# Kernel tuning notes

Measured on AMD Instinct MI355X. Metric: run time of the kernel, lower is better.

Reference implementation:

```python
import jax, jax.numpy as jnp
import numpy as np

B, N, E = 64, 2048, 32768
F_IN, NHID, RULES = 256, 512, 128
RATIO = 0.5
K1 = int(np.ceil(RATIO * N)); K2 = int(np.ceil(RATIO * K1)); K3 = int(np.ceil(RATIO * K2))


def _gcn(x, src, dst, em, W, b):
    # GCNConv with self-loops and symmetric normalization; em is a float edge-validity mask.
    n = x.shape[0]
    h = x @ W  # [n, out]
    deg = jax.ops.segment_sum(em, dst, num_segments=n) + 1.0  # in-degree + self-loop
    dinv = jax.lax.rsqrt(deg)
    coef = dinv[src] * dinv[dst] * em  # [E]
    agg = jax.ops.segment_sum(h[src] * coef[:, None], dst, num_segments=n)
    return agg + h / deg[:, None] + b  # second term = self-loop with norm 1/deg


def _sag_pool(x, src, dst, em, Wg, bg, k):
    # SAGPooling: GCN scorer, per-graph top-k, scale kept nodes by tanh(score), filter+reindex edges.
    n = x.shape[0]
    score = _gcn(x, src, dst, em, Wg, bg)[:, 0]  # [n]
    vals, perm = jax.lax.top_k(score, k)
    xk = x[perm] * jnp.tanh(vals)[:, None]  # [k, F]
    newidx = jnp.full((n,), -1, dtype=src.dtype).at[perm].set(jnp.arange(k, dtype=src.dtype))
    ns, nd = newidx[src], newidx[dst]
    keep = em * (ns >= 0).astype(em.dtype) * (nd >= 0).astype(em.dtype)
    return xk, jnp.maximum(ns, 0), jnp.maximum(nd, 0), keep


_gcn_b = jax.vmap(_gcn, in_axes=(0, 0, 0, 0, None, None))
_pool_b = jax.vmap(_sag_pool, in_axes=(0, 0, 0, 0, None, None, None))


def setup_inputs() -> dict:
    key = jax.random.key(0)
    ks = jax.random.split(key, 16)
    def w(k, shape, fan_in):
        return jax.random.normal(k, shape, jnp.float32) * (1.0 / np.sqrt(fan_in))
    return {
        "x": jax.random.normal(ks[0], (B, N, F_IN), jnp.float32),
        "src": jax.random.randint(ks[1], (B, E), 0, N, jnp.int32),
        "dst": jax.random.randint(ks[2], (B, E), 0, N, jnp.int32),
        "W1": w(ks[3], (F_IN, NHID), F_IN), "b1": jnp.zeros((NHID,), jnp.float32),
        "Wp1": w(ks[4], (NHID, 1), NHID), "bp1": jnp.zeros((1,), jnp.float32),
        "W2": w(ks[5], (NHID, NHID), NHID), "b2": jnp.zeros((NHID,), jnp.float32),
        "Wp2": w(ks[6], (NHID, 1), NHID), "bp2": jnp.zeros((1,), jnp.float32),
        "W3": w(ks[7], (NHID, NHID), NHID), "b3": jnp.zeros((NHID,), jnp.float32),
        "Wp3": w(ks[8], (NHID, 1), NHID), "bp3": jnp.zeros((1,), jnp.float32),
        "lin1_W": w(ks[9], (2 * NHID, NHID), 2 * NHID), "lin1_b": jnp.zeros((NHID,), jnp.float32),
        "lin2_W": w(ks[10], (NHID, NHID // 2), NHID), "lin2_b": jnp.zeros((NHID // 2,), jnp.float32),
        "pi_W": w(ks[11], (NHID // 2, RULES), NHID // 2), "pi_b": jnp.zeros((RULES,), jnp.float32),
        "v_W": w(ks[12], (NHID // 2, 1), NHID // 2), "v_b": jnp.zeros((1,), jnp.float32),
    }


def reference(x, src, dst, W1, b1, Wp1, bp1, W2, b2, Wp2, bp2, W3, b3, Wp3, bp3,
              lin1_W, lin1_b, lin2_W, lin2_b, pi_W, pi_b, v_W, v_b):
    em = jnp.ones(src.shape, x.dtype)
    h = jax.nn.relu(_gcn_b(x, src, dst, em, W1, b1))
    h, s, d, em = _pool_b(h, src, dst, em, Wp1, bp1, K1)
    x1 = jnp.concatenate([h.max(axis=1), h.mean(axis=1)], axis=1)  # [B, 2*NHID]
    h = jax.nn.relu(_gcn_b(h, s, d, em, W2, b2))
    h, s, d, em = _pool_b(h, s, d, em, Wp2, bp2, K2)
    x2 = jnp.concatenate([h.max(axis=1), h.mean(axis=1)], axis=1)
    h = jax.nn.relu(_gcn_b(h, s, d, em, W3, b3))
    h, s, d, em = _pool_b(h, s, d, em, Wp3, bp3, K3)
    x3 = jnp.concatenate([h.max(axis=1), h.mean(axis=1)], axis=1)
    z = x1 + x2 + x3
    z = jax.nn.relu(z @ lin1_W + lin1_b)
    z = jax.nn.relu(z @ lin2_W + lin2_b)
    pi = jax.nn.log_softmax(z @ pi_W + pi_b, axis=1)
    v = jax.nn.relu(z @ v_W + v_b)
    return pi, v
```

## Files before the change

kernel.cpp:

```cpp
#include <hip/hip_runtime.h>
#include <math.h>
#include <cstdint>

#define B_   64
#define N_   2048
#define E_   32768
#define FIN  256
#define H_   512

typedef __bf16 bf16x8 __attribute__((ext_vector_type(8)));
typedef float  f32x4  __attribute__((ext_vector_type(4)));

__device__ __forceinline__ unsigned short f2bf(float f) {
  unsigned u = __float_as_uint(f);
  u += 0x7FFF + ((u >> 16) & 1);
  return (unsigned short)(u >> 16);
}
__device__ __forceinline__ unsigned pk2(float a, float b) {
  return (unsigned)f2bf(a) | ((unsigned)f2bf(b) << 16);
}
__device__ __forceinline__ float bflo(unsigned u) { return __uint_as_float(u << 16); }
__device__ __forceinline__ float bfhi(unsigned u) { return __uint_as_float(u & 0xFFFF0000u); }

__device__ __forceinline__ void accum8(float* acc, uint4 u, float c) {
  acc[0] += c * bflo(u.x); acc[1] += c * bfhi(u.x);
  acc[2] += c * bflo(u.y); acc[3] += c * bfhi(u.y);
  acc[4] += c * bflo(u.z); acc[5] += c * bfhi(u.z);
  acc[6] += c * bflo(u.w); acc[7] += c * bfhi(u.w);
}

__device__ __forceinline__ void glds16(const void* g, void* l) {
  __builtin_amdgcn_global_load_lds(
      (const __attribute__((address_space(1))) unsigned int*)g,
      (__attribute__((address_space(3))) unsigned int*)l, 16, 0, 0);
}

__global__ void xcvt_k(const float* __restrict__ x, unsigned short* __restrict__ xb) {
  int i = blockIdx.x * 256 + threadIdx.x;
  float4 f = reinterpret_cast<const float4*>(x)[i];
  uint2 o; o.x = pk2(f.x, f.y); o.y = pk2(f.z, f.w);
  reinterpret_cast<uint2*>(xb)[i] = o;
}

__global__ void wcvt_k(const float* __restrict__ W, unsigned short* __restrict__ Wt, int K) {
  int idx = blockIdx.x * 256 + threadIdx.x;
  int k = idx >> 9, n = idx & 511;
  Wt[n * K + k] = f2bf(W[idx]);
}

__global__ __launch_bounds__(256) void gemm_mfma(
    const unsigned short* __restrict__ Xb,
    const int* __restrict__ perm, const float* __restrict__ tanhv,
    const unsigned short* __restrict__ Wt, unsigned short* __restrict__ Y,
    int K, int kl2, int nsl2,
    const float* __restrict__ bias, const float* __restrict__ wp, float* __restrict__ hs) {
  __shared__ uint4 As[512];
  __shared__ uint4 Bs[512];
  const int tid = threadIdx.x;
  const int w = tid >> 6, L = tid & 63;
  const int bid = blockIdx.x;
  const int xcd = bid & 7;
  const int t = bid >> 3;
  const int colb = t & 3;
  const int strip = ((t >> 2) << 3) + xcd;
  const int m0 = strip * 128;
  const int n0 = colb * 128;
  const int e = L & 15, q = L >> 4;

  const int sw3 = (L >> 3) & 7;
  const int cA = (w * 64 + L) ^ sw3;
  const int rloc = cA >> 2;
  const int kcs = (cA & 3) * 8;

  f32x4 acc[4][4];
#pragma unroll
  for (int j = 0; j < 4; j++)
#pragma unroll
    for (int nn = 0; nn < 4; nn++) acc[j][nn] = (f32x4){0.f, 0.f, 0.f, 0.f};

  size_t asrc[2];
#pragma unroll
  for (int i = 0; i < 2; i++) {
    int g = m0 + i * 64 + rloc;
    size_t row;
    if (perm) {
      int b = g >> kl2;
      int node = perm[g];
      row = (size_t)(b << nsl2) + node;
    } else {
      row = (size_t)g;
    }
    asrc[i] = row * (size_t)K + kcs;
  }
  size_t bsrc[2];
#pragma unroll
  for (int i = 0; i < 2; i++) bsrc[i] = (size_t)(n0 + i * 64 + rloc) * K + kcs;

  const int fo = e * 4 + q;
  const int fosw = fo ^ (fo >> 3);

  for (int k0 = 0; k0 < K; k0 += 32) {
    glds16(Xb + asrc[0] + k0, &As[0 * 256 + w * 64]);
    glds16(Xb + asrc[1] + k0, &As[1 * 256 + w * 64]);
    glds16(Wt + bsrc[0] + k0, &Bs[0 * 256 + w * 64]);
    glds16(Wt + bsrc[1] + k0, &Bs[1 * 256 + w * 64]);
    __syncthreads();
    bf16x8 af[4], bfr[4];
#pragma unroll
    for (int j = 0; j < 4; j++) af[j]  = __builtin_bit_cast(bf16x8, As[((w & 1) * 4 + j) * 64 + fosw]);
#pragma unroll
    for (int j = 0; j < 4; j++) bfr[j] = __builtin_bit_cast(bf16x8, Bs[((w >> 1) * 4 + j) * 64 + fosw]);
#pragma unroll
    for (int j = 0; j < 4; j++)
#pragma unroll
      for (int nn = 0; nn < 4; nn++)
        acc[j][nn] = __builtin_amdgcn_mfma_f32_16x16x32_bf16(af[j], bfr[nn], acc[j][nn], 0, 0, 0);
    __syncthreads();
  }
  float bs[4], wsv[4];
#pragma unroll
  for (int nn = 0; nn < 4; nn++) {
    int coly = n0 + ((w >> 1) * 4 + nn) * 16 + e;
    bs[nn]  = bias ? bias[coly] : 0.f;
    wsv[nn] = wp ? wp[coly] : 0.f;
  }
#pragma unroll
  for (int j = 0; j < 4; j++) {
    int mt = (w & 1) * 4 + j;
#pragma unroll
    for (int r = 0; r < 4; r++) {
      int grow = m0 + mt * 16 + q * 4 + r;
      float t2 = tanhv ? tanhv[grow] : 1.0f;
      float p = 0.f;
#pragma unroll
      for (int nn = 0; nn < 4; nn++) {
        int coly = n0 + ((w >> 1) * 4 + nn) * 16 + e;
        float v = acc[j][nn][r] * t2;
        if (bias) v = fmaxf(v + bs[nn], 0.f);
        Y[(size_t)grow * 512 + coly] = f2bf(v);
        p += v * wsv[nn];
      }
      if (wp) {
        p += __shfl_xor(p, 1, 64); p += __shfl_xor(p, 2, 64);
        p += __shfl_xor(p, 4, 64); p += __shfl_xor(p, 8, 64);
        if ((L & 15) == 0) atomicAdd(&hs[grow], p);
      }
    }
  }
}

__global__ void count_k(const int* __restrict__ dst, int* __restrict__ cnt, int nl2) {
  int g = blockIdx.x * 256 + threadIdx.x;
  int d = dst[g];
  if (d < 0) return;
  int b = g >> 15;
  atomicAdd(&cnt[(b << nl2) + d], 1);
}

__global__ __launch_bounds__(256) void scan_k(const int* __restrict__ cnt,
                                              int* __restrict__ rowptr, int* __restrict__ cursor,
                                              float* __restrict__ deg, float* __restrict__ dinv, int n) {
  int b = blockIdx.x, tid = threadIdx.x;
  __shared__ int ls[2048];
  __shared__ int ch[256];
  int per = n >> 8;
  int base = tid * per;
  int s = 0;
  for (int i = 0; i < per; i++) { int v = cnt[b * n + base + i]; ls[base + i] = v; s += v; }
  ch[tid] = s;
  __syncthreads();
  for (int off = 1; off < 256; off <<= 1) {
    int v = (tid >= off) ? ch[tid - off] : 0;
    __syncthreads();
    ch[tid] += v;
    __syncthreads();
  }
  int run = (tid == 0) ? 0 : ch[tid - 1];
  for (int i = 0; i < per; i++) {
    int v = ls[base + i];
    rowptr[b * (n + 1) + base + i] = run;
    cursor[b * n + base + i] = run;
    float d = (float)(v + 1);
    deg[b * n + base + i] = d;
    dinv[b * n + base + i] = 1.0f / sqrtf(d);
    run += v;
  }
  if (tid == 255) rowptr[b * (n + 1) + n] = run;
}

__global__ void fill_k(const int* __restrict__ src, const int* __restrict__ dst,
                       const float* __restrict__ dinv, int* cursor, int* col,
                       float* ce, int nl2) {
  int g = blockIdx.x * 256 + threadIdx.x;
  int d = dst[g];
  if (d < 0) return;
  int b = g >> 15;
  int s = src[g];
  int pos = atomicAdd(&cursor[(b << nl2) + d], 1);
  col[(b << 15) + pos] = s;
  ce[(b << 15) + pos] = dinv[(b << nl2) + s] * dinv[(b << nl2) + d];
}

__global__ __launch_bounds__(256) void aggx_k(
    const unsigned short* __restrict__ X,
    const int* __restrict__ rowptr, const int* __restrict__ col,
    const float* __restrict__ ce, const float* __restrict__ deg,
    unsigned short* __restrict__ Xa) {
  const int w = threadIdx.x >> 6, L = threadIdx.x & 63;
  const int xcd = blockIdx.x & 7;
  const int slot = blockIdx.x >> 3;
  const int gslot = slot >> 9;
  const int v4 = slot & 511;
  const int b = (gslot << 3) + xcd;
  const int v = v4 * 4 + w;
  const int bbase = b << 11;
  const int vg = bbase + v;
  const int rb = b * (N_ + 1) + v;
  const int st = rowptr[rb], en = rowptr[rb + 1];
  const int* cb = col + (b << 15);
  const float* cee = ce + (b << 15);
  const int h = L >> 5, hl = L & 31;
  const unsigned short* Xb_ = X + (size_t)bbase * 256 + hl * 8;
  const int T = en - st + 1;
  const float selfc = 1.0f / deg[vg];
  float acc[8] = {0.f, 0.f, 0.f, 0.f, 0.f, 0.f, 0.f, 0.f};
  for (int t = h; t < T; t += 2) {
    bool isE = (t < T - 1);
    int s = isE ? cb[st + t] : v;
    float c = isE ? cee[st + t] : selfc;
    uint4 u = *(const uint4*)(Xb_ + (size_t)s * 256);
    accum8(acc, u, c);
  }
#pragma unroll
  for (int i = 0; i < 8; i++) acc[i] += __shfl_xor(acc[i], 32, 64);
  if (h == 0) {
    uint4 o;
    o.x = pk2(acc[0], acc[1]); o.y = pk2(acc[2], acc[3]);
    o.z = pk2(acc[4], acc[5]); o.w = pk2(acc[6], acc[7]);
    *(uint4*)(Xa + (size_t)vg * 256 + hl * 8) = o;
  }
}

template <int NL2>
__global__ __launch_bounds__(256) void agg_k(
    const unsigned short* __restrict__ H,
    const int* __restrict__ rowptr, const int* __restrict__ col,
    const float* __restrict__ ce, const float* __restrict__ deg,
    const float* __restrict__ bias, const float* __restrict__ wp,
    unsigned short* __restrict__ C, float* __restrict__ hs) {
  const int n = 1 << NL2;
  const int xcd = blockIdx.x & 7;
  const int slot = blockIdx.x >> 3;
  const int gslot = slot >> (NL2 - 2);
  const int v4 = slot & ((1 << (NL2 - 2)) - 1);
  const int b = (gslot << 3) + xcd;
  const int w = threadIdx.x >> 6, L = threadIdx.x & 63;
  const int v = v4 * 4 + w;
  const int bbase = b << NL2;
  const int vg = bbase + v;
  const int rb = b * (n + 1) + v;
  const int st = rowptr[rb], en = rowptr[rb + 1];
  const int* cb = col + (b << 15);
  const float* cee = ce + (b << 15);
  const unsigned short* Hb_ = H + (size_t)bbase * 512 + (size_t)L * 8;

  float acc[8] = {0.f, 0.f, 0.f, 0.f, 0.f, 0.f, 0.f, 0.f};
  int e2 = st;
  for (; e2 + 4 <= en; e2 += 4) {
    int s0 = cb[e2], s1 = cb[e2 + 1], s2 = cb[e2 + 2], s3 = cb[e2 + 3];
    float c0 = cee[e2], c1 = cee[e2 + 1], c2 = cee[e2 + 2], c3 = cee[e2 + 3];
    uint4 u0 = *(const uint4*)(Hb_ + (size_t)s0 * 512);
    uint4 u1 = *(const uint4*)(Hb_ + (size_t)s1 * 512);
    uint4 u2 = *(const uint4*)(Hb_ + (size_t)s2 * 512);
    uint4 u3 = *(const uint4*)(Hb_ + (size_t)s3 * 512);
    accum8(acc, u0, c0); accum8(acc, u1, c1);
    accum8(acc, u2, c2); accum8(acc, u3, c3);
  }
  for (; e2 < en; e2++) {
    int s = cb[e2];
    uint4 u = *(const uint4*)(Hb_ + (size_t)s * 512);
    accum8(acc, u, cee[e2]);
  }
  {
    float idg = 1.0f / deg[vg];
    uint4 u = *(const uint4*)(Hb_ + (size_t)v * 512);
    accum8(acc, u, idg);
  }
  float4 bLo = *(const float4*)(bias + L * 8);
  float4 bHi = *(const float4*)(bias + L * 8 + 4);
  acc[0] = fmaxf(acc[0] + bLo.x, 0.f); acc[1] = fmaxf(acc[1] + bLo.y, 0.f);
  acc[2] = fmaxf(acc[2] + bLo.z, 0.f); acc[3] = fmaxf(acc[3] + bLo.w, 0.f);
  acc[4] = fmaxf(acc[4] + bHi.x, 0.f); acc[5] = fmaxf(acc[5] + bHi.y, 0.f);
  acc[6] = fmaxf(acc[6] + bHi.z, 0.f); acc[7] = fmaxf(acc[7] + bHi.w, 0.f);
  uint4 o;
  o.x = pk2(acc[0], acc[1]); o.y = pk2(acc[2], acc[3]);
  o.z = pk2(acc[4], acc[5]); o.w = pk2(acc[6], acc[7]);
  *(uint4*)(C + (size_t)vg * 512 + L * 8) = o;
  float4 wLo = *(const float4*)(wp + L * 8);
  float4 wHi = *(const float4*)(wp + L * 8 + 4);
  float p = acc[0] * wLo.x + acc[1] * wLo.y + acc[2] * wLo.z + acc[3] * wLo.w
          + acc[4] * wHi.x + acc[5] * wHi.y + acc[6] * wHi.z + acc[7] * wHi.w;
#pragma unroll
  for (int off = 32; off > 0; off >>= 1) p += __shfl_down(p, off, 64);
  if (L == 0) hs[vg] = p;
}

__global__ void scoreagg_k(const float* __restrict__ hs, const int* __restrict__ rowptr,
                           const int* __restrict__ col, const float* __restrict__ ce,
                           const float* __restrict__ deg, const float* __restrict__ bp,
                           float* __restrict__ score, int nl2) {
  int idx = blockIdx.x * 256 + threadIdx.x;
  int n = 1 << nl2;
  int b = idx >> nl2, v = idx & (n - 1);
  int rb = b * (n + 1) + v;
  int st = rowptr[rb], en = rowptr[rb + 1];
  const int* cb = col + (b << 15);
  const float* cee = ce + (b << 15);
  int bbase = b << nl2;
  float acc = 0.f;
  int e = st;
  for (; e + 4 <= en; e += 4) {
    acc += hs[bbase + cb[e]] * cee[e] + hs[bbase + cb[e + 1]] * cee[e + 1]
         + hs[bbase + cb[e + 2]] * cee[e + 2] + hs[bbase + cb[e + 3]] * cee[e + 3];
  }
  for (; e < en; e++) acc += hs[bbase + cb[e]] * cee[e];
  score[idx] = acc + hs[idx] / deg[idx] + bp[0];
}

__global__ __launch_bounds__(1024) void topk_k(const float* __restrict__ score, int* __restrict__ perm,
                                               float* __restrict__ tanhv, int* __restrict__ newidx,
                                               int n, int k) {
  int b = blockIdx.x, tid = threadIdx.x;
  __shared__ float ss[2048];
  __shared__ int si[2048];
  for (int i = tid; i < n; i += 1024) { ss[i] = score[b * n + i]; si[i] = i; }
  __syncthreads();
  for (int size = 2; size <= n; size <<= 1) {
    for (int stride = size >> 1; stride > 0; stride >>= 1) {
      for (int i = tid; i < n; i += 1024) {
        int j = i ^ stride;
        if (j > i) {
          bool up = ((i & size) == 0);
          float fi = ss[i], fj = ss[j];
          int ii = si[i], ij = si[j];
          bool iBefore = (fi > fj) || (fi == fj && ii < ij);
          bool sw = up ? (!iBefore) : iBefore;
          if (sw) { ss[i] = fj; ss[j] = fi; si[i] = ij; si[j] = ii; }
        }
      }
      __syncthreads();
    }
  }
  for (int r = tid; r < n; r += 1024) newidx[b * n + si[r]] = (r < k) ? r : -1;
  for (int r = tid; r < k; r += 1024) { perm[b * k + r] = si[r]; tanhv[b * k + r] = tanhf(ss[r]); }
}

__global__ void reindex_count_k(const int* srcO, const int* dstO, const int* newidx,
                                int* srcN, int* dstN, int* cnt, int nl2new) {
  int g = blockIdx.x * 256 + threadIdx.x;
  int b = g >> 15;
  int dd = dstO[g];
  int sN = 0, dN = -1;
  if (dd >= 0) {
    int ns = newidx[(b << (nl2new + 1)) + srcO[g]];
    int nd = newidx[(b << (nl2new + 1)) + dd];
    if (ns >= 0 && nd >= 0) {
      sN = ns; dN = nd;
      atomicAdd(&cnt[(b << nl2new) + nd], 1);
    }
  }
  srcN[g] = sN; dstN[g] = dN;
}

__global__ __launch_bounds__(512) void statsp_k(const unsigned short* __restrict__ C,
    const int* __restrict__ perm, const float* __restrict__ tv,
    float* __restrict__ zp, int nsl2, int k, int kch) {
  int b = blockIdx.x, rg = blockIdx.y, f = threadIdx.x;
  int r0 = rg * kch;
  float mx = -1e30f, sm = 0.f;
#pragma unroll 4
  for (int r = r0; r < r0 + kch; r++) {
    int node = perm[b * k + r];
    float t = tv[b * k + r];
    float val = __uint_as_float((unsigned)C[((size_t)((b << nsl2) + node)) * 512 + f] << 16) * t;
    mx = fmaxf(mx, val); sm += val;
  }
  zp[(size_t)(b * 8 + rg) * 1024 + f] = mx;
  zp[(size_t)(b * 8 + rg) * 1024 + 512 + f] = sm;
}

__global__ __launch_bounds__(512) void statsr_k(const float* __restrict__ zp,
                                                float* __restrict__ z, int k) {
  int b = blockIdx.x, f = threadIdx.x;
  float mx = -1e30f, sm = 0.f;
#pragma unroll
  for (int g = 0; g < 8; g++) {
    mx = fmaxf(mx, zp[(size_t)(b * 8 + g) * 1024 + f]);
    sm += zp[(size_t)(b * 8 + g) * 1024 + 512 + f];
  }
  z[b * 1024 + f] += mx;
  z[b * 1024 + 512 + f] += sm / (float)k;
}

__global__ __launch_bounds__(256) void mlp_k(const float* __restrict__ z, const float* __restrict__ W1,
                                             const float* __restrict__ b1, const float* __restrict__ W2,
                                             const float* __restrict__ b2, const float* __restrict__ piW,
                                             const float* __restrict__ pib, const float* __restrict__ vW,
                                             const float* __restrict__ vb, float* __restrict__ out) {
  int b = blockIdx.x, tid = threadIdx.x;
  __shared__ float zr[1024];
  __shared__ float z1[512];
  __shared__ float z2[256];
  __shared__ float pl[128];
  __shared__ float red[2];
  for (int i = tid; i < 1024; i += 256) zr[i] = z[b * 1024 + i];
  __syncthreads();
  for (int o = tid; o < 512; o += 256) {
    float a = b1[o];
    for (int i = 0; i < 1024; i++) a += zr[i] * W1[i * 512 + o];
    z1[o] = fmaxf(a, 0.f);
  }
  __syncthreads();
  {
    int o = tid;
    float a = b2[o];
    for (int i = 0; i < 512; i++) a += z1[i] * W2[i * 256 + o];
    z2[o] = fmaxf(a, 0.f);
  }
  __syncthreads();
  if (tid < 128) {
    float a = pib[tid];
    for (int i = 0; i < 256; i++) a += z2[i] * piW[i * 128 + tid];
    pl[tid] = a;
  }
  __syncthreads();
  if (tid == 0) {
    float m = -1e30f;
    for (int i = 0; i < 128; i++) m = fmaxf(m, pl[i]);
    float se = 0.f;
    for (int i = 0; i < 128; i++) se += expf(pl[i] - m);
    red[0] = m; red[1] = logf(se);
    float a = vb[0];
    for (int i = 0; i < 256; i++) a += z2[i] * vW[i];
    out[B_ * 128 + b] = fmaxf(a, 0.f);
  }
  __syncthreads();
  if (tid < 128) out[b * 128 + tid] = pl[tid] - red[0] - red[1];
}

extern "C" void kernel_launch(void* const* d_in, const int* in_sizes, int n_in,
                              void* d_out, int out_size, void* d_ws, size_t ws_size,
                              hipStream_t stream) {
  const float* x    = (const float*)d_in[0];
  const int*   src0 = (const int*)d_in[1];
  const int*   dst0 = (const int*)d_in[2];
  const float* W1   = (const float*)d_in[3];
  const float* b1   = (const float*)d_in[4];
  const float* Wp1  = (const float*)d_in[5];
  const float* bp1  = (const float*)d_in[6];
  const float* W2   = (const float*)d_in[7];
  const float* b2   = (const float*)d_in[8];
  const float* Wp2  = (const float*)d_in[9];
  const float* bp2  = (const float*)d_in[10];
  const float* W3   = (const float*)d_in[11];
  const float* b3   = (const float*)d_in[12];
  const float* Wp3  = (const float*)d_in[13];
  const float* bp3  = (const float*)d_in[14];
  const float* l1W  = (const float*)d_in[15];
  const float* l1b  = (const float*)d_in[16];
  const float* l2W  = (const float*)d_in[17];
  const float* l2b  = (const float*)d_in[18];
  const float* piW  = (const float*)d_in[19];
  const float* pib  = (const float*)d_in[20];
  const float* vW   = (const float*)d_in[21];
  const float* vb   = (const float*)d_in[22];
  float* out = (float*)d_out;
  (void)in_sizes; (void)n_in; (void)out_size; (void)ws_size;

  unsigned short* Cb = (unsigned short*)d_in[0];

  char* base = (char*)d_ws;
  size_t off = 0;
  auto alloc = [&](size_t bytes) -> void* {
    void* r = base + off;
    off += (bytes + 255) & ~(size_t)255;
    return r;
  };
  unsigned short* Hb   = (unsigned short*)alloc((size_t)B_ * 1024 * H_ * 2);
  unsigned short* xb   = (unsigned short*)alloc((size_t)B_ * N_ * FIN * 2);
  unsigned short* Xa   = (unsigned short*)alloc((size_t)B_ * N_ * FIN * 2);
  unsigned short* W1t  = (unsigned short*)alloc((size_t)512 * 256 * 2);
  unsigned short* W2t  = (unsigned short*)alloc((size_t)512 * 512 * 2);
  unsigned short* W3t  = (unsigned short*)alloc((size_t)512 * 512 * 2);
  int*   srcA   = (int*)alloc((size_t)B_ * E_ * 4);
  int*   dstA   = (int*)alloc((size_t)B_ * E_ * 4);
  int*   col    = (int*)alloc((size_t)B_ * E_ * 4);
  float* coefE  = (float*)alloc((size_t)B_ * E_ * 4);
  int*   cnt    = (int*)alloc((size_t)B_ * N_ * 4);
  int*   cursor = (int*)alloc((size_t)B_ * N_ * 4);
  int*   rowptr = (int*)alloc((size_t)B_ * (N_ + 1) * 4);
  float* deg    = (float*)alloc((size_t)B_ * N_ * 4);
  float* dinv   = (float*)alloc((size_t)B_ * N_ * 4);
  float* hs     = (float*)alloc((size_t)B_ * N_ * 4);
  float* score  = (float*)alloc((size_t)B_ * N_ * 4);
  int*   newidx = (int*)alloc((size_t)B_ * N_ * 4);
  int*   perm   = (int*)alloc((size_t)B_ * 1024 * 4);
  float* tanhv  = (float*)alloc((size_t)B_ * 1024 * 4);
  float* zpart  = (float*)alloc((size_t)B_ * 8 * 1024 * 4);
  float* z      = (float*)alloc((size_t)B_ * 1024 * 4);

  const int EB = B_ * E_ / 256;

  xcvt_k<<<B_ * N_ * FIN / 4 / 256, 256, 0, stream>>>(x, xb);
  wcvt_k<<<256 * 512 / 256, 256, 0, stream>>>(W1, W1t, 256);
  wcvt_k<<<512 * 512 / 256, 256, 0, stream>>>(W2, W2t, 512);
  wcvt_k<<<512 * 512 / 256, 256, 0, stream>>>(W3, W3t, 512);
  hipMemsetAsync(z, 0, (size_t)B_ * 1024 * 4, stream);

  {
    hipMemsetAsync(cnt, 0, (size_t)B_ * 2048 * 4, stream);
    count_k<<<EB, 256, 0, stream>>>(dst0, cnt, 11);
    scan_k<<<B_, 256, 0, stream>>>(cnt, rowptr, cursor, deg, dinv, 2048);
    fill_k<<<EB, 256, 0, stream>>>(src0, dst0, dinv, cursor, col, coefE, 11);
    aggx_k<<<B_ * 2048 / 4, 256, 0, stream>>>(xb, rowptr, col, coefE, deg, Xa);
    hipMemsetAsync(hs, 0, (size_t)B_ * 2048 * 4, stream);
    gemm_mfma<<<B_ * 2048 / 128 * 4, 256, 0, stream>>>(
        Xa, nullptr, nullptr, W1t, Cb, 256, 0, 0, b1, Wp1, hs);
    scoreagg_k<<<B_ * 2048 / 256, 256, 0, stream>>>(hs, rowptr, col, coefE, deg, bp1, score, 11);
    topk_k<<<B_, 1024, 0, stream>>>(score, perm, tanhv, newidx, 2048, 1024);
    statsp_k<<<dim3(B_, 8), 512, 0, stream>>>(Cb, perm, tanhv, zpart, 11, 1024, 128);
    statsr_k<<<B_, 512, 0, stream>>>(zpart, z, 1024);
    hipMemsetAsync(cnt, 0, (size_t)B_ * 1024 * 4, stream);
    reindex_count_k<<<EB, 256, 0, stream>>>(src0, dst0, newidx, srcA, dstA, cnt, 10);
    scan_k<<<B_, 256, 0, stream>>>(cnt, rowptr, cursor, deg, dinv, 1024);
    fill_k<<<EB, 256, 0, stream>>>(srcA, dstA, dinv, cursor, col, coefE, 10);
  }
  {
    gemm_mfma<<<B_ * 1024 / 128 * 4, 256, 0, stream>>>(
        Cb, perm, tanhv, W2t, Hb, 512, 10, 11, nullptr, nullptr, nullptr);
    agg_k<10><<<B_ * 1024 / 4, 256, 0, stream>>>(Hb, rowptr, col, coefE, deg, b2, Wp2, Cb, hs);
    scoreagg_k<<<B_ * 1024 / 256, 256, 0, stream>>>(hs, rowptr, col, coefE, deg, bp2, score, 10);
    topk_k<<<B_, 1024, 0, stream>>>(score, perm, tanhv, newidx, 1024, 512);
    statsp_k<<<dim3(B_, 8), 512, 0, stream>>>(Cb, perm, tanhv, zpart, 10, 512, 64);
    statsr_k<<<B_, 512, 0, stream>>>(zpart, z, 512);
    hipMemsetAsync(cnt, 0, (size_t)B_ * 512 * 4, stream);
    reindex_count_k<<<EB, 256, 0, stream>>>(srcA, dstA, newidx, srcA, dstA, cnt, 9);
    scan_k<<<B_, 256, 0, stream>>>(cnt, rowptr, cursor, deg, dinv, 512);
    fill_k<<<EB, 256, 0, stream>>>(srcA, dstA, dinv, cursor, col, coefE, 9);
  }
  {
    gemm_mfma<<<B_ * 512 / 128 * 4, 256, 0, stream>>>(
        Cb, perm, tanhv, W3t, Hb, 512, 9, 10, nullptr, nullptr, nullptr);
    agg_k<9><<<B_ * 512 / 4, 256, 0, stream>>>(Hb, rowptr, col, coefE, deg, b3, Wp3, Cb, hs);
    scoreagg_k<<<B_ * 512 / 256, 256, 0, stream>>>(hs, rowptr, col, coefE, deg, bp3, score, 9);
    topk_k<<<B_, 1024, 0, stream>>>(score, perm, tanhv, newidx, 512, 256);
    statsp_k<<<dim3(B_, 8), 512, 0, stream>>>(Cb, perm, tanhv, zpart, 9, 256, 32);
    statsr_k<<<B_, 512, 0, stream>>>(zpart, z, 256);
  }

  mlp_k<<<B_, 256, 0, stream>>>(z, l1W, l1b, l2W, l2b, piW, pib, vW, vb, out);
}
```

Baseline: 1.106 ms.

## Split MLP head into split-K kernels and use warp-shuffle softmax reduction

Replaces the single 64-block MLP head kernel with three kernels. The first two spread the lin1 and lin2 matrix-vector products over more blocks using split-K partial sums. The final kernel computes log-softmax and the value head with wavefront shuffle reductions instead of a serial single-thread loop. The aim is better GPU occupancy for a latency-bound tail stage, at the cost of two extra launches and round trips of partial sums through global memory.

```diff
diff --git a/kernel.cpp b/kernel.cpp
--- a/kernel.cpp
+++ b/kernel.cpp
@@ -402,50 +402,87 @@
   z[b * 1024 + 512 + f] += sm / (float)k;
 }
 
-__global__ __launch_bounds__(256) void mlp_k(const float* __restrict__ z, const float* __restrict__ W1,
-                                             const float* __restrict__ b1, const float* __restrict__ W2,
-                                             const float* __restrict__ b2, const float* __restrict__ piW,
-                                             const float* __restrict__ pib, const float* __restrict__ vW,
-                                             const float* __restrict__ vb, float* __restrict__ out) {
-  int b = blockIdx.x, tid = threadIdx.x;
-  __shared__ float zr[1024];
-  __shared__ float z1[512];
-  __shared__ float z2[256];
-  __shared__ float pl[128];
-  __shared__ float red[2];
-  for (int i = tid; i < 1024; i += 256) zr[i] = z[b * 1024 + i];
+__global__ __launch_bounds__(256) void mlp1_k(const float* __restrict__ z,
+                                              const float* __restrict__ W1,
+                                              float* __restrict__ zp1) {
+  const int kc = blockIdx.x & 7;
+  const int b = blockIdx.x >> 3;
+  const int tid = threadIdx.x;
+  __shared__ float zs[128];
+  if (tid < 128) zs[tid] = z[b * 1024 + kc * 128 + tid];
   __syncthreads();
-  for (int o = tid; o < 512; o += 256) {
-    float a = b1[o];
-    for (int i = 0; i < 1024; i++) a += zr[i] * W1[i * 512 + o];
-    z1[o] = fmaxf(a, 0.f);
+  float a0 = 0.f, a1 = 0.f;
+  const float* Wb = W1 + (size_t)(kc * 128) * 512 + tid * 2;
+#pragma unroll 4
+  for (int i = 0; i < 128; i++) {
+    float2 w = *(const float2*)(Wb + (size_t)i * 512);
+    float zi = zs[i];
+    a0 += zi * w.x; a1 += zi * w.y;
+  }
+  reinterpret_cast<float2*>(zp1 + ((size_t)(kc * 64 + b)) * 512)[tid] = make_float2(a0, a1);
+}
+
+__global__ __launch_bounds__(256) void mlp2_k(const float* __restrict__ zp1,
+                                              const float* __restrict__ b1,
+                                              const float* __restrict__ W2,
+                                              float* __restrict__ zp2) {
+  const int kc = blockIdx.x & 1;
+  const int b = blockIdx.x >> 1;
+  const int tid = threadIdx.x;
+  __shared__ float z1s[256];
+  {
+    int i = kc * 256 + tid;
+    float a = b1[i];
+#pragma unroll
+    for (int g = 0; g < 8; g++) a += zp1[((size_t)(g * 64 + b)) * 512 + i];
+    z1s[tid] = fmaxf(a, 0.f);
   }
   __syncthreads();
-  {
-    int o = tid;
-    float a = b2[o];
-    for (int i = 0; i < 512; i++) a += z1[i] * W2[i * 256 + o];
-    z2[o] = fmaxf(a, 0.f);
+  float a = 0.f;
+  const float* Wb = W2 + (size_t)(kc * 256) * 256 + tid;
+#pragma unroll 4
+  for (int i = 0; i < 256; i++) a += z1s[i] * Wb[(size_t)i * 256];
+  zp2[((size_t)(kc * 64 + b)) * 256 + tid] = a;
+}
+
+__global__ __launch_bounds__(128) void mlp3_k(const float* __restrict__ zp2,
+                                              const float* __restrict__ b2,
+                                              const float* __restrict__ piW,
+                                              const float* __restrict__ pib,
+                                              const float* __restrict__ vW,
+                                              const float* __restrict__ vb,
+                                              float* __restrict__ out) {
+  const int b = blockIdx.x, tid = threadIdx.x;
+  __shared__ float z2s[256];
+  __shared__ float wred[4];
+  __shared__ float sred[2];
+  for (int t = tid; t < 256; t += 128) {
+    float a = b2[t] + zp2[(size_t)b * 256 + t] + zp2[(size_t)(64 + b) * 256 + t];
+    z2s[t] = fmaxf(a, 0.f);
   }
   __syncthreads();
-  if (tid < 128) {
-    float a = pib[tid];
-    for (int i = 0; i < 256; i++) a += z2[i] * piW[i * 128 + tid];
-    pl[tid] = a;
-  }
+  float a = pib[tid];
+#pragma unroll 4
+  for (int i = 0; i < 256; i++) a += z2s[i] * piW[(size_t)i * 128 + tid];
+  float vp = z2s[tid] * vW[tid] + z2s[tid + 128] * vW[tid + 128];
+  float m = a;
+#pragma unroll
+  for (int off = 32; off > 0; off >>= 1) {
+    vp += __shfl_xor(vp, off, 64);
+    m = fmaxf(m, __shfl_xor(m, off, 64));
+  }
+  const int wv = tid >> 6;
+  if ((tid & 63) == 0) { wred[wv] = m; wred[2 + wv] = vp; }
   __syncthreads();
-  if (tid == 0) {
-    float m = -1e30f;
-    for (int i = 0; i < 128; i++) m = fmaxf(m, pl[i]);
-    float se = 0.f;
-    for (int i = 0; i < 128; i++) se += expf(pl[i] - m);
-    red[0] = m; red[1] = logf(se);
-    float a = vb[0];
-    for (int i = 0; i < 256; i++) a += z2[i] * vW[i];
-    out[B_ * 128 + b] = fmaxf(a, 0.f);
-  }
+  m = fmaxf(wred[0], wred[1]);
+  float s = expf(a - m);
+#pragma unroll
+  for (int off = 32; off > 0; off >>= 1) s += __shfl_xor(s, off, 64);
+  if ((tid & 63) == 0) sred[wv] = s;
   __syncthreads();
-  if (tid < 128) out[b * 128 + tid] = pl[tid] - red[0] - red[1];
+  s = sred[0] + sred[1];
+  if (tid == 0) out[B_ * 128 + b] = fmaxf(vb[0] + wred[2] + wred[3], 0.f);
+  out[b * 128 + tid] = a - m - logf(s);
 }
 
 extern "C" void kernel_launch(void* const* d_in, const int* in_sizes, int n_in,
@@ -509,6 +546,9 @@
   float* zpart  = (float*)alloc((size_t)B_ * 8 * 1024 * 4);
   float* z      = (float*)alloc((size_t)B_ * 1024 * 4);
 
+  float* zp1 = zpart;
+  float* zp2 = zpart + (size_t)8 * 64 * 512;
+
   const int EB = B_ * E_ / 256;
 
   xcvt_k<<<B_ * N_ * FIN / 4 / 256, 256, 0, stream>>>(x, xb);
@@ -558,5 +598,7 @@
     statsr_k<<<B_, 512, 0, stream>>>(zpart, z, 256);
   }
 
-  mlp_k<<<B_, 256, 0, stream>>>(z, l1W, l1b, l2W, l2b, piW, pib, vW, vb, out);
-}
+  mlp1_k<<<B_ * 8, 256, 0, stream>>>(z, l1W, zp1);
+  mlp2_k<<<B_ * 2, 256, 0, stream>>>(zp1, l1b, l2W, zp2);
+  mlp3_k<<<B_, 128, 0, stream>>>(zp2, l2b, piW, pib, vW, vb, out);
+}
```

New measurement: 1.070 ms. 1.03x faster.
